# Kernel optimization log

Measured on AMD Instinct MI355X. Metric: run time of the kernel, lower is better.

The kernel has to match this reference:

```python
import jax, jax.numpy as jnp
import numpy as np

B, LT, D, N, H = 16, 512, 1024, 4096, 16
LN_EPS = 1e-5


def setup_inputs() -> dict:
    key = jax.random.key(0)
    ks = jax.random.split(key, 10)
    s = 0.02
    struct_token = jax.random.normal(ks[0], (N, D), dtype=jnp.float32)
    text_token = jax.random.normal(ks[1], (B, LT, D), dtype=jnp.float32)
    # contiguous, sorted segment ids: 256 struct tokens per batch element
    struct_batch = jnp.repeat(jnp.arange(B, dtype=jnp.int32), N // B)
    return {
        "struct_token": struct_token,
        "text_token": text_token,
        "in_proj_w": jax.random.normal(ks[2], (3 * D, D), dtype=jnp.float32) * s,
        "in_proj_b": jnp.zeros((3 * D,), jnp.float32),
        "attn_out_w": jax.random.normal(ks[3], (D, D), dtype=jnp.float32) * s,
        "attn_out_b": jnp.zeros((D,), jnp.float32),
        "ln_g": jnp.ones((D,), jnp.float32),
        "ln_b": jnp.zeros((D,), jnp.float32),
        "proj_w": jax.random.normal(ks[4], (D, D), dtype=jnp.float32) * s,
        "proj_b": jnp.zeros((D,), jnp.float32),
        "struct_batch": struct_batch,
        "L_max": N // B,
    }


def reference(struct_token, text_token, in_proj_w, in_proj_b, attn_out_w,
              attn_out_b, ln_g, ln_b, proj_w, proj_b, struct_batch, L_max):
    Bq = text_token.shape[0]
    Dm = struct_token.shape[-1]
    dh = Dm // H
    Ntok = struct_token.shape[0]

    # ---- ragged pad-pack (struct_batch is sorted/contiguous per segment) ----
    counts = jnp.bincount(struct_batch, length=Bq)                 # [B]
    starts = jnp.concatenate([jnp.zeros((1,), counts.dtype),
                              jnp.cumsum(counts)[:-1]])            # [B]
    pos = jnp.arange(Ntok) - starts[struct_batch]                  # [N] position in segment
    padded = jnp.zeros((Bq, L_max, Dm), struct_token.dtype)
    padded = padded.at[struct_batch, pos].set(struct_token)        # [B, Ls, D]

    # ---- nn.MultiheadAttention (batch_first): Q=padded, K=V=text ----
    wq, wk, wv = in_proj_w[:Dm], in_proj_w[Dm:2 * Dm], in_proj_w[2 * Dm:]
    bq, bk, bv = in_proj_b[:Dm], in_proj_b[Dm:2 * Dm], in_proj_b[2 * Dm:]
    q = (padded @ wq.T + bq).reshape(Bq, L_max, H, dh)
    k = (text_token @ wk.T + bk).reshape(Bq, -1, H, dh)
    v = (text_token @ wv.T + bv).reshape(Bq, -1, H, dh)
    scores = jnp.einsum('bqhd,bkhd->bhqk', q, k) / jnp.sqrt(jnp.float32(dh))
    attn = jax.nn.softmax(scores, axis=-1)
    ctx = jnp.einsum('bhqk,bkhd->bqhd', attn, v).reshape(Bq, L_max, Dm)
    fused = ctx @ attn_out_w.T + attn_out_b                        # [B, Ls, D]

    # ---- LayerNorm + output projection ----
    mu = fused.mean(-1, keepdims=True)
    var = fused.var(-1, keepdims=True)
    fused = (fused - mu) * jax.lax.rsqrt(var + LN_EPS) * ln_g + ln_b
    fused = fused @ proj_w.T + proj_b

    # ---- unpack valid tokens + scatter-mean over segments ----
    tok = fused[struct_batch, pos]                                 # [N, D]
    seg_sum = jax.ops.segment_sum(tok, struct_batch, num_segments=Bq)
    return seg_sum / jnp.maximum(counts, 1)[:, None].astype(seg_sum.dtype)
```

## Files before the change

### kernel.cpp

```cpp
#include <hip/hip_runtime.h>

constexpr int B  = 16;
constexpr int LT = 512;
constexpr int D  = 1024;
constexpr int N  = 4096;
constexpr int H  = 16;
constexpr int DH = D / H;
constexpr int LMAX = N / B;
constexpr float LN_EPS = 1e-5f;

typedef short  s16x8 __attribute__((ext_vector_type(8)));
typedef float  f32x4 __attribute__((ext_vector_type(4)));

__device__ __forceinline__ unsigned short f2bf(float x) {
    unsigned int u = __float_as_uint(x);
    unsigned int r = (u + 0x7fffu + ((u >> 16) & 1u)) >> 16;
    return (unsigned short)r;
}
__device__ __forceinline__ float bf2f(unsigned short u) {
    return __uint_as_float((unsigned int)u << 16);
}

__device__ __forceinline__ void load_lds16(const void* g, void* l) {
    __builtin_amdgcn_global_load_lds(
        (const __attribute__((address_space(1))) unsigned int*)g,
        (__attribute__((address_space(3))) unsigned int*)l, 16, 0, 0);
}

__global__ __launch_bounds__(256) void cast3_prep(
        const float* __restrict__ x0, unsigned short* __restrict__ y0, int n0,
        const float* __restrict__ x1, unsigned short* __restrict__ y1, int n1,
        const float* __restrict__ x2, unsigned short* __restrict__ y2, int n2,
        const int* __restrict__ sb, int* __restrict__ counts, int* __restrict__ starts) {
    __shared__ int s_counts[B];
    int t = threadIdx.x;
    if (blockIdx.x == 6144) {
        if (t < B) s_counts[t] = 0;
        __syncthreads();
        for (int i = t; i < N; i += 256) atomicAdd(&s_counts[sb[i]], 1);
        __syncthreads();
        if (t == 0) {
            int run = 0;
            for (int b = 0; b < B; b++) { starts[b] = run; run += s_counts[b]; }
        }
        if (t < B) counts[t] = s_counts[t];
        return;
    }
    long long i = (long long)(blockIdx.x * 256 + t) * 8;
    const float* x; unsigned short* y;
    if (i < n0)                { x = x0 + i; y = y0 + i; }
    else if (i < (long long)n0 + n1) { long long j = i - n0; x = x1 + j; y = y1 + j; }
    else if (i < (long long)n0 + n1 + n2) { long long j = i - n0 - n1; x = x2 + j; y = y2 + j; }
    else return;
    float4 a = *(const float4*)x;
    float4 b = *(const float4*)(x + 4);
    ushort4 o1, o2;
    o1.x = f2bf(a.x); o1.y = f2bf(a.y); o1.z = f2bf(a.z); o1.w = f2bf(a.w);
    o2.x = f2bf(b.x); o2.y = f2bf(b.y); o2.z = f2bf(b.z); o2.w = f2bf(b.w);
    *(ushort4*)y = o1;
    *(ushort4*)(y + 4) = o2;
}

__global__ void scatter_full(const float* __restrict__ st,
                             const int* __restrict__ counts,
                             const int* __restrict__ starts,
                             unsigned short* __restrict__ padded) {
    int p = blockIdx.x, b = blockIdx.y;
    int d = threadIdx.x * 4;
    size_t off = ((size_t)(b * LMAX + p)) * D + d;
    ushort4 o = {0, 0, 0, 0};
    if (p < counts[b]) {
        float4 v = *(const float4*)&st[(size_t)(starts[b] + p) * D + d];
        o.x = f2bf(v.x); o.y = f2bf(v.y); o.z = f2bf(v.z); o.w = f2bf(v.w);
    }
    *(ushort4*)&padded[off] = o;
}

template<typename Epi>
__device__ __forceinline__ void gemm32(const unsigned short* __restrict__ A,
                                       const unsigned short* __restrict__ W,
                                       int K, int kbeg, int kend, int m0, int n0,
                                       unsigned short* __restrict__ As,
                                       unsigned short* __restrict__ Bs,
                                       Epi&& epi) {
    const int tid  = threadIdx.x;
    const int lane = tid & 63;
    const int wid  = tid >> 6;
    const int wr   = wid >> 1;
    const int wc   = wid & 1;
    const int fm   = lane & 15;
    const int quad = lane >> 4;
    const int NK   = (kend - kbeg) >> 5;

    f32x4 acc[4][4];
#pragma unroll
    for (int i = 0; i < 4; i++)
#pragma unroll
        for (int j = 0; j < 4; j++) acc[i][j] = (f32x4){0.f, 0.f, 0.f, 0.f};

    const int rA0 = tid >> 2,          sA0 = (tid & 3) ^ (rA0 & 3);
    const int rA1 = (tid + 512) >> 2,  sA1 = (tid & 3) ^ (rA1 & 3);
    const int rB  = tid >> 2,          sB  = (tid & 3) ^ (rB & 3);
    const unsigned short* gA0 = A + (size_t)(m0 + rA0) * K + kbeg + sA0 * 8;
    const unsigned short* gA1 = A + (size_t)(m0 + rA1) * K + kbeg + sA1 * 8;
    const unsigned short* gB  = W + (size_t)(n0 + rB ) * K + kbeg + sB  * 8;
    unsigned short* lA0 = As + (size_t)tid * 8;
    unsigned short* lA1 = As + (size_t)(tid + 512) * 8;
    unsigned short* lB  = Bs + (size_t)tid * 8;

    const int sl8 = (quad ^ (fm & 3)) * 8;
    int offA[4], offB[4];
#pragma unroll
    for (int i = 0; i < 4; i++) offA[i] = (wr * 64 + i * 16 + fm) * 32 + sl8;
#pragma unroll
    for (int j = 0; j < 4; j++) offB[j] = (wc * 64 + j * 16 + fm) * 32 + sl8;

    load_lds16(gA0, lA0);
    load_lds16(gA1, lA1);
    load_lds16(gB , lB );

    for (int s = 0; s < NK; s++) {
        const int go = (s + 1) << 5;
        const int ab = (s & 1) << 13;
        const int bb = (s & 1) << 12;
        asm volatile("s_barrier" ::: "memory");
        if (s + 1 < NK) {
            const int ab2 = ((s + 1) & 1) << 13;
            const int bb2 = ((s + 1) & 1) << 12;
            load_lds16(gA0 + go, lA0 + ab2);
            load_lds16(gA1 + go, lA1 + ab2);
            load_lds16(gB  + go, lB  + bb2);
            asm volatile("s_waitcnt vmcnt(3)" ::: "memory");
        } else {
            asm volatile("s_waitcnt vmcnt(0)" ::: "memory");
        }
        asm volatile("s_barrier" ::: "memory");

        s16x8 af[4], bf[4];
#pragma unroll
        for (int i = 0; i < 4; i++) af[i] = *(const s16x8*)&As[ab + offA[i]];
#pragma unroll
        for (int j = 0; j < 4; j++) bf[j] = *(const s16x8*)&Bs[bb + offB[j]];

        __builtin_amdgcn_s_setprio(1);
#pragma unroll
        for (int i = 0; i < 4; i++)
#pragma unroll
            for (int j = 0; j < 4; j++)
                acc[i][j] = __builtin_amdgcn_mfma_f32_16x16x32_bf16(af[i], bf[j], acc[i][j], 0, 0, 0);
        __builtin_amdgcn_s_setprio(0);
    }

    const int fr = quad * 4;
#pragma unroll
    for (int i = 0; i < 4; i++)
#pragma unroll
        for (int j = 0; j < 4; j++) {
            int row = m0 + wr * 64 + i * 16 + fr;
            int col = n0 + wc * 64 + j * 16 + fm;
#pragma unroll
            for (int r = 0; r < 4; r++)
                epi(row + r, col, acc[i][j][r]);
        }
}

__global__ __launch_bounds__(512, 4) void qkv_fused(const unsigned short* __restrict__ padded,
                                                    const unsigned short* __restrict__ text,
                                                    const unsigned short* __restrict__ wqkv,
                                                    const float* __restrict__ bqkv,
                                                    unsigned short* __restrict__ qpack,
                                                    unsigned short* __restrict__ kpack,
                                                    unsigned short* __restrict__ vpack) {
    __shared__ __align__(16) unsigned short As[2 * 8192];
    __shared__ __align__(16) unsigned short Bs[2 * 4096];
    int orig = blockIdx.x;
    int id = (orig & 7) * 80 + (orig >> 3);
    if (id < 128) {
        int mt = id >> 3, nt = id & 7;
        gemm32(padded, wqkv, D, 0, D, mt * 256, nt * 128, As, Bs,
            [&](int mm, int col, float v) {
                float val = v + bqkv[col];
                int b = mm >> 8, q = mm & 255;
                int h = col >> 6, d = col & 63;
                qpack[(size_t)(b * H + h) * 16384 + (d >> 3) * 2048 + q * 8 + (d & 7)] = f2bf(val);
            });
    } else if (id < 384) {
        int f = id - 128;
        int mt = f >> 3, nt = f & 7;
        gemm32(text, wqkv + (size_t)D * D, D, 0, D, mt * 256, nt * 128, As, Bs,
            [&](int mm, int col, float v) {
                float val = v + bqkv[D + col];
                int b = mm >> 9, key = mm & 511;
                int h = col >> 6, d = col & 63;
                kpack[(size_t)(b * H + h) * 32768 + (d >> 3) * 4096 + key * 8 + (d & 7)] = f2bf(val);
            });
    } else {
        int f = id - 384;
        int mt = f >> 6, nt = f & 63;
        gemm32(wqkv + 2 * (size_t)D * D, text, D, 0, D, mt * 256, nt * 128, As, Bs,
            [&](int mm, int col, float v) {
                float val = v + bqkv[2 * D + mm];
                int h = mm >> 6, d = mm & 63;
                int b = col >> 9, key = col & 511;
                vpack[(size_t)(b * H + h) * 32768 + (key >> 3) * 512 + d * 8 + (key & 7)] = f2bf(val);
            });
    }
}

__global__ __launch_bounds__(512, 4) void gemm_bf2(const unsigned short* __restrict__ A,
                                                   const unsigned short* __restrict__ W,
                                                   unsigned short* __restrict__ C0,
                                                   unsigned short* __restrict__ C1,
                                                   int Nn, int K) {
    __shared__ __align__(16) unsigned short As[2 * 8192];
    __shared__ __align__(16) unsigned short Bs[2 * 4096];
    int orig = blockIdx.x;
    int id = (orig & 7) * 32 + (orig >> 3);
    int kh = id >> 7;
    int f  = id & 127;
    int mt = f >> 3, nt = f & 7;
    unsigned short* C = kh ? C1 : C0;
    gemm32(A, W, K, kh * 512, (kh + 1) * 512, mt * 256, nt * 128, As, Bs,
        [&](int mm, int col, float v) {
            C[(size_t)mm * Nn + col] = f2bf(v);
        });
}

constexpr int PKW = 72;

__global__ __launch_bounds__(512) void attn_mfma(const unsigned short* __restrict__ qpack,
                                                 const unsigned short* __restrict__ kpack,
                                                 const unsigned short* __restrict__ vpack,
                                                 unsigned short* __restrict__ ctx) {
    __shared__ __align__(16) unsigned short KV[16384];
    __shared__ __align__(16) unsigned short Ps[8 * 16 * PKW];

    const int tid = threadIdx.x;
    const int lane = tid & 63;
    const int wv = tid >> 6;
    const int fm = lane & 15;
    const int quad = lane >> 4;
    const int h = blockIdx.x, b = blockIdx.y, half = blockIdx.z;
    const int q0 = half * 128 + wv * 16;

    const unsigned short* qp = qpack + (size_t)(b * H + h) * 16384;
    const unsigned short* kp = kpack + (size_t)(b * H + h) * 32768;
    const unsigned short* vp = vpack + (size_t)(b * H + h) * 32768;

    const s16x8 aq0 = *(const s16x8*)&qp[quad * 2048 + (q0 + fm) * 8];
    const s16x8 aq1 = *(const s16x8*)&qp[(4 + quad) * 2048 + (q0 + fm) * 8];

    f32x4 sc[32];

    for (int kc = 0; kc < 2; kc++) {
        __syncthreads();
#pragma unroll
        for (int it = 0; it < 4; it++) {
            int f = it * 512 + tid;
            load_lds16(kp + (f >> 8) * 4096 + kc * 2048 + (f & 255) * 8, KV + f * 8);
        }
        __syncthreads();
#pragma unroll
        for (int t = 0; t < 16; t++) {
            s16x8 bk0 = *(const s16x8*)&KV[quad * 2048 + (t * 16 + fm) * 8];
            s16x8 bk1 = *(const s16x8*)&KV[(4 + quad) * 2048 + (t * 16 + fm) * 8];
            f32x4 a = (f32x4){0.f, 0.f, 0.f, 0.f};
            a = __builtin_amdgcn_mfma_f32_16x16x32_bf16(aq0, bk0, a, 0, 0, 0);
            a = __builtin_amdgcn_mfma_f32_16x16x32_bf16(aq1, bk1, a, 0, 0, 0);
            sc[kc * 16 + t] = a;
        }
    }

    const float scale = 0.125f;
    float mx[4], l[4], inv[4];
#pragma unroll
    for (int r = 0; r < 4; r++) {
        float m = sc[0][r];
#pragma unroll
        for (int t = 1; t < 32; t++) m = fmaxf(m, sc[t][r]);
        mx[r] = m;
    }
#pragma unroll
    for (int o = 1; o < 16; o <<= 1)
#pragma unroll
        for (int r = 0; r < 4; r++) mx[r] = fmaxf(mx[r], __shfl_xor(mx[r], o));
#pragma unroll
    for (int r = 0; r < 4; r++) l[r] = 0.f;
#pragma unroll
    for (int t = 0; t < 32; t++)
#pragma unroll
        for (int r = 0; r < 4; r++) {
            float e = __expf((sc[t][r] - mx[r]) * scale);
            sc[t][r] = e;
            l[r] += e;
        }
#pragma unroll
    for (int o = 1; o < 16; o <<= 1)
#pragma unroll
        for (int r = 0; r < 4; r++) l[r] += __shfl_xor(l[r], o);
#pragma unroll
    for (int r = 0; r < 4; r++) inv[r] = 1.f / l[r];

    f32x4 co[4];
#pragma unroll
    for (int n = 0; n < 4; n++) co[n] = (f32x4){0.f, 0.f, 0.f, 0.f};
    unsigned short* Pw = Ps + wv * (16 * PKW);

    for (int vc = 0; vc < 2; vc++) {
        __syncthreads();
#pragma unroll
        for (int it = 0; it < 4; it++) {
            int f = it * 512 + tid;
            load_lds16(vp + vc * 16384 + f * 8, KV + f * 8);
        }
        __syncthreads();
        for (int cs = 0; cs < 4; cs++) {
            int c = vc * 4 + cs;
#pragma unroll
            for (int tt = 0; tt < 4; tt++)
#pragma unroll
                for (int r = 0; r < 4; r++)
                    Pw[(quad * 4 + r) * PKW + tt * 16 + fm] = f2bf(sc[c * 4 + tt][r]);
#pragma unroll
            for (int s = 0; s < 2; s++) {
                s16x8 ap = *(const s16x8*)&Pw[fm * PKW + s * 32 + quad * 8];
#pragma unroll
                for (int n = 0; n < 4; n++) {
                    s16x8 bv = *(const s16x8*)&KV[(cs * 8 + s * 4 + quad) * 512 + (n * 16 + fm) * 8];
                    co[n] = __builtin_amdgcn_mfma_f32_16x16x32_bf16(ap, bv, co[n], 0, 0, 0);
                }
            }
        }
    }

    const size_t obase = (size_t)(b * LMAX + q0) * D + h * DH;
#pragma unroll
    for (int n = 0; n < 4; n++)
#pragma unroll
        for (int r = 0; r < 4; r++)
            ctx[obase + (size_t)(quad * 4 + r) * D + n * 16 + fm] = f2bf(co[n][r] * inv[r]);
}

__global__ __launch_bounds__(256) void lnmean_kernel(const unsigned short* __restrict__ f1a,
                                                     const unsigned short* __restrict__ f1b,
                                                     const float* __restrict__ bo,
                                                     const float* __restrict__ g,
                                                     const float* __restrict__ bb,
                                                     const int* __restrict__ counts,
                                                     float* __restrict__ msum) {
    int b = blockIdx.x;
    int t = threadIdx.x;
    int wv = t >> 6, lane = t & 63;
    int cnt = counts[b];
    int s0 = blockIdx.y * 32 + wv * 8;
    int s1 = min(cnt, s0 + 8);

    float4 gg[4], bv[4], bo4[4];
#pragma unroll
    for (int c = 0; c < 4; c++) {
        gg[c]  = *(const float4*)&g[c * 256 + lane * 4];
        bv[c]  = *(const float4*)&bb[c * 256 + lane * 4];
        bo4[c] = *(const float4*)&bo[c * 256 + lane * 4];
    }
    float4 acc[4];
#pragma unroll
    for (int c = 0; c < 4; c++) acc[c] = (float4){0.f, 0.f, 0.f, 0.f};

    for (int s = s0; s < s1; s++) {
        size_t rbase = ((size_t)(b * LMAX + s)) * D;
        float4 v[4];
        float sm = 0.f, ss = 0.f;
#pragma unroll
        for (int c = 0; c < 4; c++) {
            ushort4 ua = *(const ushort4*)&f1a[rbase + c * 256 + lane * 4];
            ushort4 ub = *(const ushort4*)&f1b[rbase + c * 256 + lane * 4];
            v[c].x = bf2f(ua.x) + bf2f(ub.x) + bo4[c].x;
            v[c].y = bf2f(ua.y) + bf2f(ub.y) + bo4[c].y;
            v[c].z = bf2f(ua.z) + bf2f(ub.z) + bo4[c].z;
            v[c].w = bf2f(ua.w) + bf2f(ub.w) + bo4[c].w;
            sm += v[c].x + v[c].y + v[c].z + v[c].w;
            ss += v[c].x * v[c].x + v[c].y * v[c].y + v[c].z * v[c].z + v[c].w * v[c].w;
        }
#pragma unroll
        for (int o = 32; o; o >>= 1) { sm += __shfl_xor(sm, o); ss += __shfl_xor(ss, o); }
        float mu = sm * (1.f / D);
        float var = ss * (1.f / D) - mu * mu;
        float r = rsqrtf(var + LN_EPS);
#pragma unroll
        for (int c = 0; c < 4; c++) {
            acc[c].x += (v[c].x - mu) * r * gg[c].x + bv[c].x;
            acc[c].y += (v[c].y - mu) * r * gg[c].y + bv[c].y;
            acc[c].z += (v[c].z - mu) * r * gg[c].z + bv[c].z;
            acc[c].w += (v[c].w - mu) * r * gg[c].w + bv[c].w;
        }
    }
    float inv = 1.f / (float)max(cnt, 1);
#pragma unroll
    for (int c = 0; c < 4; c++) {
        int base = b * D + c * 256 + lane * 4;
        atomicAdd(&msum[base + 0], acc[c].x * inv);
        atomicAdd(&msum[base + 1], acc[c].y * inv);
        atomicAdd(&msum[base + 2], acc[c].z * inv);
        atomicAdd(&msum[base + 3], acc[c].w * inv);
    }
}

__global__ __launch_bounds__(256) void tproj_kernel(const float* __restrict__ msum,
                                                    const float* __restrict__ W,
                                                    const float* __restrict__ bias,
                                                    float* __restrict__ out) {
    int lane = threadIdx.x & 63;
    int n = blockIdx.x * 4 + (threadIdx.x >> 6);
    float4 wr[4];
#pragma unroll
    for (int i = 0; i < 4; i++)
        wr[i] = *(const float4*)&W[(size_t)n * D + i * 256 + lane * 4];
    float bn = bias[n];
    for (int b = 0; b < B; b++) {
        float s = 0.f;
#pragma unroll
        for (int i = 0; i < 4; i++) {
            float4 m4 = *(const float4*)&msum[(size_t)b * D + i * 256 + lane * 4];
            s += m4.x * wr[i].x + m4.y * wr[i].y + m4.z * wr[i].z + m4.w * wr[i].w;
        }
#pragma unroll
        for (int o = 32; o; o >>= 1) s += __shfl_xor(s, o);
        if (lane == 0) out[(size_t)b * D + n] = s + bn;
    }
}

extern "C" void kernel_launch(void* const* d_in, const int* in_sizes, int n_in,
                              void* d_out, int out_size, void* d_ws, size_t ws_size,
                              hipStream_t stream) {
    const float* struct_token = (const float*)d_in[0];
    const float* text_token   = (const float*)d_in[1];
    const float* in_proj_w    = (const float*)d_in[2];
    const float* in_proj_b    = (const float*)d_in[3];
    const float* attn_out_w   = (const float*)d_in[4];
    const float* attn_out_b   = (const float*)d_in[5];
    const float* ln_g         = (const float*)d_in[6];
    const float* ln_b         = (const float*)d_in[7];
    const float* proj_w       = (const float*)d_in[8];
    const float* proj_b       = (const float*)d_in[9];
    const int*   sb           = (const int*)d_in[10];
    float* out = (float*)d_out;

    const size_t MQ  = (size_t)B * LMAX;
    const size_t MKV = (size_t)B * LT;

    char* p = (char*)d_ws;
    unsigned short* padded_b = (unsigned short*)p;  p += MQ * D * 2;
    unsigned short* text_b   = (unsigned short*)p;  p += MKV * D * 2;
    unsigned short* wqkv_b   = (unsigned short*)p;  p += (size_t)3 * D * D * 2;
    unsigned short* wattn_b  = (unsigned short*)p;  p += (size_t)D * D * 2;
    unsigned short* qpack    = (unsigned short*)p;  p += MQ * D * 2;
    unsigned short* kpack    = (unsigned short*)p;  p += MKV * D * 2;
    unsigned short* vpack    = (unsigned short*)p;  p += MKV * D * 2;
    unsigned short* ctx_b    = (unsigned short*)p;  p += MQ * D * 2;
    unsigned short* f1a      = (unsigned short*)p;  p += MQ * D * 2;
    unsigned short* f1b      = (unsigned short*)p;  p += MQ * D * 2;
    float* msum = (float*)p;  p += (size_t)B * D * 4;
    int* counts = (int*)p;  p += B * 4;
    int* starts = (int*)p;  p += B * 4;

    hipMemsetAsync(msum, 0, (size_t)B * D * 4, stream);

    cast3_prep<<<6145, 256, 0, stream>>>(
        text_token, text_b, (int)(MKV * D),
        in_proj_w,  wqkv_b, 3 * D * D,
        attn_out_w, wattn_b, D * D,
        sb, counts, starts);

    scatter_full<<<dim3(LMAX, B), 256, 0, stream>>>(struct_token, counts, starts, padded_b);

    qkv_fused<<<640, 512, 0, stream>>>(padded_b, text_b, wqkv_b, in_proj_b,
                                       qpack, kpack, vpack);

    attn_mfma<<<dim3(H, B, 2), 512, 0, stream>>>(qpack, kpack, vpack, ctx_b);

    gemm_bf2<<<256, 512, 0, stream>>>(ctx_b, wattn_b, f1a, f1b, D, D);

    lnmean_kernel<<<dim3(B, 8), 256, 0, stream>>>(f1a, f1b, attn_out_b, ln_g, ln_b, counts, msum);

    tproj_kernel<<<256, 256, 0, stream>>>(msum, proj_w, proj_b, out);
}
```

Before: 261.0 us.

## Triple-buffer GEMM LDS tiles and change swizzle pattern

Moves the shared bf16 GEMM mainloop from double to triple buffering. Global-to-LDS loads are now issued two k-steps ahead, with the vmcnt waits adjusted to match. The XOR swizzle for LDS placement now uses bits 3-4 of the chunk index and (fm>>1) on the read side, to reduce LDS bank conflicts. LDS per block grows from 48KB to 72KB, which may lower the number of resident blocks per CU.

```diff
diff --git a/kernel.cpp b/kernel.cpp
--- a/kernel.cpp
+++ b/kernel.cpp
@@ -98,17 +98,17 @@
 #pragma unroll
         for (int j = 0; j < 4; j++) acc[i][j] = (f32x4){0.f, 0.f, 0.f, 0.f};
 
-    const int rA0 = tid >> 2,          sA0 = (tid & 3) ^ (rA0 & 3);
-    const int rA1 = (tid + 512) >> 2,  sA1 = (tid & 3) ^ (rA1 & 3);
-    const int rB  = tid >> 2,          sB  = (tid & 3) ^ (rB & 3);
+    const int rA0 = tid >> 2,          sA0 = (tid & 3) ^ ((tid >> 3) & 3);
+    const int cA1 = tid + 512;
+    const int rA1 = cA1 >> 2,          sA1 = (cA1 & 3) ^ ((cA1 >> 3) & 3);
     const unsigned short* gA0 = A + (size_t)(m0 + rA0) * K + kbeg + sA0 * 8;
     const unsigned short* gA1 = A + (size_t)(m0 + rA1) * K + kbeg + sA1 * 8;
-    const unsigned short* gB  = W + (size_t)(n0 + rB ) * K + kbeg + sB  * 8;
+    const unsigned short* gB  = W + (size_t)(n0 + rA0) * K + kbeg + sA0 * 8;
     unsigned short* lA0 = As + (size_t)tid * 8;
     unsigned short* lA1 = As + (size_t)(tid + 512) * 8;
     unsigned short* lB  = Bs + (size_t)tid * 8;
 
-    const int sl8 = (quad ^ (fm & 3)) * 8;
+    const int sl8 = (quad ^ ((fm >> 1) & 3)) * 8;
     int offA[4], offB[4];
 #pragma unroll
     for (int i = 0; i < 4; i++) offA[i] = (wr * 64 + i * 16 + fm) * 32 + sl8;
@@ -118,24 +118,31 @@
     load_lds16(gA0, lA0);
     load_lds16(gA1, lA1);
     load_lds16(gB , lB );
-
+    if (NK > 1) {
+        load_lds16(gA0 + 32, lA0 + 8192);
+        load_lds16(gA1 + 32, lA1 + 8192);
+        load_lds16(gB  + 32, lB  + 4096);
+    }
+
+    int buf = 0;
+    int buf2 = 2;
     for (int s = 0; s < NK; s++) {
-        const int go = (s + 1) << 5;
-        const int ab = (s & 1) << 13;
-        const int bb = (s & 1) << 12;
         asm volatile("s_barrier" ::: "memory");
-        if (s + 1 < NK) {
-            const int ab2 = ((s + 1) & 1) << 13;
-            const int bb2 = ((s + 1) & 1) << 12;
-            load_lds16(gA0 + go, lA0 + ab2);
-            load_lds16(gA1 + go, lA1 + ab2);
-            load_lds16(gB  + go, lB  + bb2);
+        if (s + 2 < NK) {
+            const int go = (s + 2) << 5;
+            load_lds16(gA0 + go, lA0 + buf2 * 8192);
+            load_lds16(gA1 + go, lA1 + buf2 * 8192);
+            load_lds16(gB  + go, lB  + buf2 * 4096);
+            asm volatile("s_waitcnt vmcnt(6)" ::: "memory");
+        } else if (s + 1 < NK) {
             asm volatile("s_waitcnt vmcnt(3)" ::: "memory");
         } else {
             asm volatile("s_waitcnt vmcnt(0)" ::: "memory");
         }
         asm volatile("s_barrier" ::: "memory");
 
+        const int ab = buf * 8192;
+        const int bb = buf * 4096;
         s16x8 af[4], bf[4];
 #pragma unroll
         for (int i = 0; i < 4; i++) af[i] = *(const s16x8*)&As[ab + offA[i]];
@@ -149,6 +156,9 @@
             for (int j = 0; j < 4; j++)
                 acc[i][j] = __builtin_amdgcn_mfma_f32_16x16x32_bf16(af[i], bf[j], acc[i][j], 0, 0, 0);
         __builtin_amdgcn_s_setprio(0);
+
+        buf  = (buf  == 2) ? 0 : buf  + 1;
+        buf2 = (buf2 == 2) ? 0 : buf2 + 1;
     }
 
     const int fr = quad * 4;
@@ -171,8 +181,8 @@
                                                     unsigned short* __restrict__ qpack,
                                                     unsigned short* __restrict__ kpack,
                                                     unsigned short* __restrict__ vpack) {
-    __shared__ __align__(16) unsigned short As[2 * 8192];
-    __shared__ __align__(16) unsigned short Bs[2 * 4096];
+    __shared__ __align__(16) unsigned short As[3 * 8192];
+    __shared__ __align__(16) unsigned short Bs[3 * 4096];
     int orig = blockIdx.x;
     int id = (orig & 7) * 80 + (orig >> 3);
     if (id < 128) {
@@ -212,8 +222,8 @@
                                                    unsigned short* __restrict__ C0,
                                                    unsigned short* __restrict__ C1,
                                                    int Nn, int K) {
-    __shared__ __align__(16) unsigned short As[2 * 8192];
-    __shared__ __align__(16) unsigned short Bs[2 * 4096];
+    __shared__ __align__(16) unsigned short As[3 * 8192];
+    __shared__ __align__(16) unsigned short Bs[3 * 4096];
     int orig = blockIdx.x;
     int id = (orig & 7) * 32 + (orig >> 3);
     int kh = id >> 7;
```

Result: no change. 257.3 us (-1.4%).

## Double-buffer K/V in attention LDS and change GEMM LDS swizzle

Applied to the files above, without the earlier changes.

The attention kernel now keeps two LDS buffers. Both K chunks are issued up front, and the V loads are issued before the softmax so they overlap with exp/sum work, with vmcnt-based waits replacing full syncthreads. The GEMM LDS XOR swizzle now keys on row bits 1-2 instead of 0-1, which targets LDS bank conflicts on fragment reads. Priority hints are added around the MFMA loops. LDS use in the attention kernel doubles to 64KB for KV, which may reduce occupancy.

```diff
diff --git a/kernel.cpp b/kernel.cpp
--- a/kernel.cpp
+++ b/kernel.cpp
@@ -98,17 +98,17 @@
 #pragma unroll
         for (int j = 0; j < 4; j++) acc[i][j] = (f32x4){0.f, 0.f, 0.f, 0.f};
 
-    const int rA0 = tid >> 2,          sA0 = (tid & 3) ^ (rA0 & 3);
-    const int rA1 = (tid + 512) >> 2,  sA1 = (tid & 3) ^ (rA1 & 3);
-    const int rB  = tid >> 2,          sB  = (tid & 3) ^ (rB & 3);
+    const int rA0 = tid >> 2,          sA0 = (tid & 3) ^ ((tid >> 3) & 3);
+    const int cA1 = tid + 512;
+    const int rA1 = cA1 >> 2,          sA1 = (cA1 & 3) ^ ((cA1 >> 3) & 3);
     const unsigned short* gA0 = A + (size_t)(m0 + rA0) * K + kbeg + sA0 * 8;
     const unsigned short* gA1 = A + (size_t)(m0 + rA1) * K + kbeg + sA1 * 8;
-    const unsigned short* gB  = W + (size_t)(n0 + rB ) * K + kbeg + sB  * 8;
+    const unsigned short* gB  = W + (size_t)(n0 + rA0) * K + kbeg + sA0 * 8;
     unsigned short* lA0 = As + (size_t)tid * 8;
     unsigned short* lA1 = As + (size_t)(tid + 512) * 8;
     unsigned short* lB  = Bs + (size_t)tid * 8;
 
-    const int sl8 = (quad ^ (fm & 3)) * 8;
+    const int sl8 = (quad ^ ((fm >> 1) & 3)) * 8;
     int offA[4], offB[4];
 #pragma unroll
     for (int i = 0; i < 4; i++) offA[i] = (wr * 64 + i * 16 + fm) * 32 + sl8;
@@ -120,11 +120,11 @@
     load_lds16(gB , lB );
 
     for (int s = 0; s < NK; s++) {
-        const int go = (s + 1) << 5;
         const int ab = (s & 1) << 13;
         const int bb = (s & 1) << 12;
         asm volatile("s_barrier" ::: "memory");
         if (s + 1 < NK) {
+            const int go = (s + 1) << 5;
             const int ab2 = ((s + 1) & 1) << 13;
             const int bb2 = ((s + 1) & 1) << 12;
             load_lds16(gA0 + go, lA0 + ab2);
@@ -136,18 +136,18 @@
         }
         asm volatile("s_barrier" ::: "memory");
 
-        s16x8 af[4], bf[4];
+        s16x8 af[4], bfv[4];
 #pragma unroll
         for (int i = 0; i < 4; i++) af[i] = *(const s16x8*)&As[ab + offA[i]];
 #pragma unroll
-        for (int j = 0; j < 4; j++) bf[j] = *(const s16x8*)&Bs[bb + offB[j]];
+        for (int j = 0; j < 4; j++) bfv[j] = *(const s16x8*)&Bs[bb + offB[j]];
 
         __builtin_amdgcn_s_setprio(1);
 #pragma unroll
         for (int i = 0; i < 4; i++)
 #pragma unroll
             for (int j = 0; j < 4; j++)
-                acc[i][j] = __builtin_amdgcn_mfma_f32_16x16x32_bf16(af[i], bf[j], acc[i][j], 0, 0, 0);
+                acc[i][j] = __builtin_amdgcn_mfma_f32_16x16x32_bf16(af[i], bfv[j], acc[i][j], 0, 0, 0);
         __builtin_amdgcn_s_setprio(0);
     }
 
@@ -232,7 +232,7 @@
                                                  const unsigned short* __restrict__ kpack,
                                                  const unsigned short* __restrict__ vpack,
                                                  unsigned short* __restrict__ ctx) {
-    __shared__ __align__(16) unsigned short KV[16384];
+    __shared__ __align__(16) unsigned short KV[2][16384];
     __shared__ __align__(16) unsigned short Ps[8 * 16 * PKW];
 
     const int tid = threadIdx.x;
@@ -250,26 +250,54 @@
     const s16x8 aq0 = *(const s16x8*)&qp[quad * 2048 + (q0 + fm) * 8];
     const s16x8 aq1 = *(const s16x8*)&qp[(4 + quad) * 2048 + (q0 + fm) * 8];
 
-    f32x4 sc[32];
-
-    for (int kc = 0; kc < 2; kc++) {
-        __syncthreads();
+#pragma unroll
+    for (int kc = 0; kc < 2; kc++)
 #pragma unroll
         for (int it = 0; it < 4; it++) {
             int f = it * 512 + tid;
-            load_lds16(kp + (f >> 8) * 4096 + kc * 2048 + (f & 255) * 8, KV + f * 8);
-        }
-        __syncthreads();
-#pragma unroll
-        for (int t = 0; t < 16; t++) {
-            s16x8 bk0 = *(const s16x8*)&KV[quad * 2048 + (t * 16 + fm) * 8];
-            s16x8 bk1 = *(const s16x8*)&KV[(4 + quad) * 2048 + (t * 16 + fm) * 8];
-            f32x4 a = (f32x4){0.f, 0.f, 0.f, 0.f};
-            a = __builtin_amdgcn_mfma_f32_16x16x32_bf16(aq0, bk0, a, 0, 0, 0);
-            a = __builtin_amdgcn_mfma_f32_16x16x32_bf16(aq1, bk1, a, 0, 0, 0);
-            sc[kc * 16 + t] = a;
-        }
-    }
+            load_lds16(kp + (f >> 8) * 4096 + kc * 2048 + (f & 255) * 8, &KV[kc][f * 8]);
+        }
+
+    f32x4 sc[32];
+
+    asm volatile("s_waitcnt vmcnt(4)" ::: "memory");
+    __builtin_amdgcn_s_barrier();
+    __builtin_amdgcn_s_setprio(1);
+#pragma unroll
+    for (int t = 0; t < 16; t++) {
+        s16x8 bk0 = *(const s16x8*)&KV[0][quad * 2048 + (t * 16 + fm) * 8];
+        s16x8 bk1 = *(const s16x8*)&KV[0][(4 + quad) * 2048 + (t * 16 + fm) * 8];
+        f32x4 a = (f32x4){0.f, 0.f, 0.f, 0.f};
+        a = __builtin_amdgcn_mfma_f32_16x16x32_bf16(aq0, bk0, a, 0, 0, 0);
+        a = __builtin_amdgcn_mfma_f32_16x16x32_bf16(aq1, bk1, a, 0, 0, 0);
+        sc[t] = a;
+    }
+    __builtin_amdgcn_s_setprio(0);
+
+    asm volatile("s_waitcnt vmcnt(0)" ::: "memory");
+    __builtin_amdgcn_s_barrier();
+    __builtin_amdgcn_s_setprio(1);
+#pragma unroll
+    for (int t = 0; t < 16; t++) {
+        s16x8 bk0 = *(const s16x8*)&KV[1][quad * 2048 + (t * 16 + fm) * 8];
+        s16x8 bk1 = *(const s16x8*)&KV[1][(4 + quad) * 2048 + (t * 16 + fm) * 8];
+        f32x4 a = (f32x4){0.f, 0.f, 0.f, 0.f};
+        a = __builtin_amdgcn_mfma_f32_16x16x32_bf16(aq0, bk0, a, 0, 0, 0);
+        a = __builtin_amdgcn_mfma_f32_16x16x32_bf16(aq1, bk1, a, 0, 0, 0);
+        sc[16 + t] = a;
+    }
+    __builtin_amdgcn_s_setprio(0);
+
+    asm volatile("s_waitcnt lgkmcnt(0)" ::: "memory");
+    __builtin_amdgcn_s_barrier();
+
+#pragma unroll
+    for (int vc = 0; vc < 2; vc++)
+#pragma unroll
+        for (int it = 0; it < 4; it++) {
+            int f = it * 512 + tid;
+            load_lds16(vp + vc * 16384 + f * 8, &KV[vc][f * 8]);
+        }
 
     const float scale = 0.125f;
     float mx[4], l[4], inv[4];
@@ -306,14 +334,14 @@
     for (int n = 0; n < 4; n++) co[n] = (f32x4){0.f, 0.f, 0.f, 0.f};
     unsigned short* Pw = Ps + wv * (16 * PKW);
 
+    asm volatile("s_waitcnt vmcnt(4)" ::: "memory");
+    __builtin_amdgcn_s_barrier();
+
     for (int vc = 0; vc < 2; vc++) {
-        __syncthreads();
-#pragma unroll
-        for (int it = 0; it < 4; it++) {
-            int f = it * 512 + tid;
-            load_lds16(vp + vc * 16384 + f * 8, KV + f * 8);
-        }
-        __syncthreads();
+        if (vc == 1) {
+            asm volatile("s_waitcnt vmcnt(0)" ::: "memory");
+            __builtin_amdgcn_s_barrier();
+        }
         for (int cs = 0; cs < 4; cs++) {
             int c = vc * 4 + cs;
 #pragma unroll
@@ -321,15 +349,17 @@
 #pragma unroll
                 for (int r = 0; r < 4; r++)
                     Pw[(quad * 4 + r) * PKW + tt * 16 + fm] = f2bf(sc[c * 4 + tt][r]);
+            __builtin_amdgcn_s_setprio(1);
 #pragma unroll
             for (int s = 0; s < 2; s++) {
                 s16x8 ap = *(const s16x8*)&Pw[fm * PKW + s * 32 + quad * 8];
 #pragma unroll
                 for (int n = 0; n < 4; n++) {
-                    s16x8 bv = *(const s16x8*)&KV[(cs * 8 + s * 4 + quad) * 512 + (n * 16 + fm) * 8];
+                    s16x8 bv = *(const s16x8*)&KV[vc][(cs * 8 + s * 4 + quad) * 512 + (n * 16 + fm) * 8];
                     co[n] = __builtin_amdgcn_mfma_f32_16x16x32_bf16(ap, bv, co[n], 0, 0, 0);
                 }
             }
+            __builtin_amdgcn_s_setprio(0);
         }
     }
 
```

After: 259.0 us. About the same (-0.8%).
